# Optimization experiments

Hardware: AMD Instinct MI355X
Metric: run time of the kernel (lower is better)

## Reference

```python
import jax, jax.numpy as jnp
import numpy as np

B, S, E, H = 4, 2048, 1024, 4
D = E // H  # head_dim = 256


def setup_inputs() -> dict:
    key = jax.random.key(0)
    ks = jax.random.split(key, 9)
    scale = 1.0 / np.sqrt(E)
    return {
        "hidden_states": jax.random.normal(ks[0], (B, S, E), jnp.float32),
        "Wq": jax.random.normal(ks[1], (E, E), jnp.float32) * scale,
        "Wk": jax.random.normal(ks[2], (E, E), jnp.float32) * scale,
        "Wv": jax.random.normal(ks[3], (E, E), jnp.float32) * scale,
        "Wo": jax.random.normal(ks[4], (E, E), jnp.float32) * scale,
        "bo": jax.random.normal(ks[5], (E,), jnp.float32) * 0.02,
        "betas": jax.random.normal(ks[6], (1, H, 1, 1), jnp.float32),
        "mem": jax.random.uniform(ks[7], (H, D, D), jnp.float32),
        "z": jax.random.uniform(ks[8], (H, D, 1), jnp.float32),
    }


def _split_heads(t):  # [B,S,E] -> [B,H,S,D]
    return t.reshape(B, S, H, D).transpose(0, 2, 1, 3)


def reference(hidden_states, Wq, Wk, Wv, Wo, bo, betas, mem, z):
    q = _split_heads(hidden_states @ Wq)  # [B,H,S,D]
    k = _split_heads(hidden_states @ Wk)
    v = _split_heads(hidden_states @ Wv)

    # linear-attention feature map (ELU + 1)
    sigma_q = jax.nn.elu(q) + 1.0
    sigma_k = jax.nn.elu(k) + 1.0

    # compressive-memory read: mem [H,D,D], z [H,D,1] broadcast over batch
    A_mem = (sigma_q @ mem) / (sigma_q @ z + 1e-6)  # [B,H,S,D]

    # standard causal softmax attention
    attn_weights = jnp.einsum("bhqd,bhkd->bhqk", q, k)
    causal = jnp.tril(jnp.ones((S, S), bool))
    mask_value = jnp.finfo(attn_weights.dtype).min
    attn_weights = jnp.where(causal, attn_weights, mask_value)
    attn_weights = jax.nn.softmax(attn_weights, axis=-1)
    attn_output = jnp.einsum("bhqk,bhkd->bhqd", attn_weights, v)

    # per-head sigmoid gate mixing memory read and local attention
    gate = jax.nn.sigmoid(betas)  # [1,H,1,1]
    attn_output = gate * A_mem + (1.0 - gate) * attn_output

    # memory update (delta rule)
    delta = (sigma_k @ mem) / (sigma_k @ z + 1e-6)  # [B,H,S,D]
    mem_new = mem + jnp.einsum("bhsd,bhse->bhde", sigma_k, v - delta)  # [B,H,D,D]
    z_new = z + sigma_k.sum(axis=-2, keepdims=True).transpose(0, 1, 3, 2)  # [B,H,D,1]

    out = attn_output.transpose(0, 2, 1, 3).reshape(B, S, E) @ Wo + bo
    return out, mem_new, z_new
```

## Files before the change

kernel.cpp:

```cpp
#include <hip/hip_runtime.h>
#include <math.h>

#define Bn 4
#define Sn 2048
#define En 1024
#define Hn 4
#define Dn 256

typedef _Float16 half8 __attribute__((ext_vector_type(8)));
typedef _Float16 half4v __attribute__((ext_vector_type(4)));
typedef float floatx4 __attribute__((ext_vector_type(4)));

#define MFMA16(a, b, c) __builtin_amdgcn_mfma_f32_16x16x32_f16((a), (b), (c), 0, 0, 0)

__device__ __forceinline__ float elup1(float x) {
    return x > 0.0f ? x + 1.0f : __expf(x);
}

__global__ void cvt_h_k(const float* __restrict__ src, _Float16* __restrict__ dst, int n4) {
    int idx = blockIdx.x * 256 + threadIdx.x;
    const int stride = gridDim.x * 256;
    for (; idx < n4; idx += stride) {
        float4 v = ((const float4*)src)[idx];
        half4v o;
        o[0] = (_Float16)v.x; o[1] = (_Float16)v.y;
        o[2] = (_Float16)v.z; o[3] = (_Float16)v.w;
        ((half4v*)dst)[idx] = o;
    }
}

__global__ __launch_bounds__(256) void trans_f32f16_k(
    const float* __restrict__ src, _Float16* __restrict__ dst, int R, int C) {
    __shared__ float T[64][65];
    const int tid = threadIdx.x;
    const int c0 = blockIdx.x * 64, r0 = blockIdx.y * 64;
    src += (size_t)blockIdx.z * R * C;
    dst += (size_t)blockIdx.z * R * C;
    {
        const int tr = tid >> 2, tc = (tid & 3) * 16;
        const float* s = src + (size_t)(r0 + tr) * C + c0 + tc;
        #pragma unroll
        for (int i = 0; i < 4; ++i) {
            float4 v = *(const float4*)(s + i * 4);
            T[tr][tc + i * 4 + 0] = v.x;
            T[tr][tc + i * 4 + 1] = v.y;
            T[tr][tc + i * 4 + 2] = v.z;
            T[tr][tc + i * 4 + 3] = v.w;
        }
    }
    __syncthreads();
    {
        const int cr = tid >> 2, rc = (tid & 3) * 16;
        half8 h0, h1;
        #pragma unroll
        for (int i = 0; i < 8; ++i) h0[i] = (_Float16)T[rc + i][cr];
        #pragma unroll
        for (int i = 0; i < 8; ++i) h1[i] = (_Float16)T[rc + 8 + i][cr];
        _Float16* d = dst + (size_t)(c0 + cr) * R + r0 + rc;
        *(half8*)d = h0;
        *(half8*)(d + 8) = h1;
    }
}

__global__ __launch_bounds__(256) void trans_h16_k(
    const _Float16* __restrict__ Vh, _Float16* __restrict__ Vtg) {
    __shared__ __align__(16) unsigned short T[64 * 72];
    const int tid = threadIdx.x;
    const int s0 = blockIdx.x * 64;
    const int e0 = blockIdx.y * 64;
    const int b = blockIdx.z;
    const int h = e0 >> 8, d0 = e0 & 255;
    {
        const int tr = tid >> 2, tc = (tid & 3) * 16;
        const _Float16* s = Vh + (size_t)(b * Sn + s0 + tr) * En + e0 + tc;
        _Float16* d = (_Float16*)T + tr * 72 + tc;
        *(half8*)d = *(const half8*)s;
        *(half8*)(d + 8) = *(const half8*)(s + 8);
    }
    __syncthreads();
    {
        const int dr = tid >> 2, sc = (tid & 3) * 16;
        const _Float16* Tp = (const _Float16*)T;
        half8 h0, h1;
        #pragma unroll
        for (int i = 0; i < 8; ++i) h0[i] = Tp[(sc + i) * 72 + dr];
        #pragma unroll
        for (int i = 0; i < 8; ++i) h1[i] = Tp[(sc + 8 + i) * 72 + dr];
        _Float16* d = Vtg + (size_t)((b * 4 + h) * 256 + d0 + dr) * (size_t)Sn + s0 + sc;
        *(half8*)d = h0;
        *(half8*)(d + 8) = h1;
    }
}

__global__ __launch_bounds__(256) void gemm16_k(
    const _Float16* __restrict__ A, const _Float16* __restrict__ Bt,
    _Float16* __restrict__ C16, float* __restrict__ C32,
    const float* __restrict__ bias) {
    __shared__ __align__(16) unsigned short Ah[128 * 40];
    __shared__ __align__(16) unsigned short Bh[128 * 40];
    const int tid = threadIdx.x;
    const int lane = tid & 63, w = tid >> 6, quad = lane >> 4, l15 = lane & 15;
    const int bm = blockIdx.y * 128, bn = blockIdx.x * 128;
    floatx4 acc[2][8];
    #pragma unroll
    for (int mt = 0; mt < 2; ++mt)
        #pragma unroll
        for (int nt = 0; nt < 8; ++nt) acc[mt][nt] = (floatx4){0.f, 0.f, 0.f, 0.f};

    const int srow = tid >> 1, skoff = (tid & 1) * 16;
    const _Float16* as = A + (size_t)(bm + srow) * 1024 + skoff;
    const _Float16* bs = Bt + (size_t)(bn + srow) * 1024 + skoff;
    _Float16* ad = (_Float16*)Ah + srow * 40 + skoff;
    _Float16* bd = (_Float16*)Bh + srow * 40 + skoff;

    for (int k0 = 0; k0 < 1024; k0 += 32) {
        if (k0) __syncthreads();
        *(half8*)ad = *(const half8*)(as + k0);
        *(half8*)(ad + 8) = *(const half8*)(as + k0 + 8);
        *(half8*)bd = *(const half8*)(bs + k0);
        *(half8*)(bd + 8) = *(const half8*)(bs + k0 + 8);
        __syncthreads();
        half8 af0 = *(const half8*)((const _Float16*)Ah + (w * 32 + l15) * 40 + quad * 8);
        half8 af1 = *(const half8*)((const _Float16*)Ah + (w * 32 + 16 + l15) * 40 + quad * 8);
        #pragma unroll
        for (int nt = 0; nt < 8; ++nt) {
            half8 bf = *(const half8*)((const _Float16*)Bh + (nt * 16 + l15) * 40 + quad * 8);
            acc[0][nt] = MFMA16(af0, bf, acc[0][nt]);
            acc[1][nt] = MFMA16(af1, bf, acc[1][nt]);
        }
    }
    #pragma unroll
    for (int mt = 0; mt < 2; ++mt)
        #pragma unroll
        for (int nt = 0; nt < 8; ++nt)
            #pragma unroll
            for (int r = 0; r < 4; ++r) {
                const int row = bm + w * 32 + mt * 16 + quad * 4 + r;
                const int col = bn + nt * 16 + l15;
                if (C16)
                    C16[(size_t)row * 1024 + col] = (_Float16)acc[mt][nt][r];
                else
                    C32[(size_t)row * 1024 + col] = acc[mt][nt][r] + bias[col];
            }
}

__global__ __launch_bounds__(256) void flash_gate_k(
    const _Float16* __restrict__ Qh, const _Float16* __restrict__ Khg,
    const _Float16* __restrict__ Vtg, const _Float16* __restrict__ memT,
    const float* __restrict__ zp, const float* __restrict__ betas,
    _Float16* __restrict__ Cmb) {
    __shared__ __align__(16) unsigned short Ksh[32 * 264];
    __shared__ __align__(16) unsigned short Vt[256 * 40];
    __shared__ __align__(16) unsigned short Pb[4 * 16 * 40];

    const int tid = threadIdx.x;
    const int lane = tid & 63;
    const int w = tid >> 6;
    const int quad = lane >> 4;
    const int l15 = lane & 15;
    const int qt = 31 - blockIdx.x;
    const int bh = blockIdx.y;
    const int b = bh >> 2;
    const int h = bh & 3;
    const int q0 = qt * 64;

    const _Float16* Qrow = Qh + (size_t)(b * Sn + q0 + w * 16 + l15) * En + h * Dn;
    half8 qf[8], sf[8];
    float denp = 0.0f;
    #pragma unroll
    for (int kc = 0; kc < 8; ++kc) {
        half8 qv = *(const half8*)(Qrow + kc * 32 + quad * 8);
        qf[kc] = qv;
        const float* zb = zp + h * Dn + kc * 32 + quad * 8;
        float4 z0 = *(const float4*)zb;
        float4 z1 = *(const float4*)(zb + 4);
        float zz[8] = {z0.x, z0.y, z0.z, z0.w, z1.x, z1.y, z1.z, z1.w};
        half8 sv;
        #pragma unroll
        for (int j = 0; j < 8; ++j) {
            float s = elup1((float)qv[j]);
            sv[j] = (_Float16)s;
            denp += s * zz[j];
        }
        sf[kc] = sv;
    }
    denp += __shfl_xor(denp, 16);
    denp += __shfl_xor(denp, 32);
    const float deninv = 1.0f / (denp + 1e-6f);
    float den4[4];
    #pragma unroll
    for (int r = 0; r < 4; ++r) den4[r] = __shfl(deninv, quad * 4 + r);

    floatx4 acc[16];
    #pragma unroll
    for (int nt = 0; nt < 16; ++nt) acc[nt] = (floatx4){0.f, 0.f, 0.f, 0.f};

    const _Float16* memh = memT + (size_t)h * 256 * 256;
    for (int dc = 0; dc < 8; ++dc) {
        __syncthreads();
        {
            const _Float16* src = memh + (size_t)tid * 256 + dc * 32;
            _Float16* dst = (_Float16*)Vt + tid * 40;
            #pragma unroll
            for (int u = 0; u < 4; ++u) *(half8*)(dst + u * 8) = *(const half8*)(src + u * 8);
        }
        __syncthreads();
        #pragma unroll
        for (int nt = 0; nt < 16; ++nt) {
            half8 bm = *(const half8*)((const _Float16*)Vt + (nt * 16 + l15) * 40 + quad * 8);
            acc[nt] = MFMA16(sf[dc], bm, acc[nt]);
        }
    }

    const float gate = 1.0f / (1.0f + __expf(-betas[h]));
    const float omg = 1.0f - gate;
    _Float16* Cb = Cmb + (size_t)(b * Sn + q0 + w * 16) * En + h * Dn;
    #pragma unroll
    for (int nt = 0; nt < 16; ++nt)
        #pragma unroll
        for (int r = 0; r < 4; ++r) {
            Cb[(size_t)(quad * 4 + r) * En + nt * 16 + l15] =
                (_Float16)(gate * acc[nt][r] * den4[r]);
            acc[nt][r] = 0.0f;
        }

    float mold[4] = {-1e30f, -1e30f, -1e30f, -1e30f};
    float lsum[4] = {0.f, 0.f, 0.f, 0.f};
    float alpha[4];
    const _Float16* Kbase = Khg + (size_t)(b * Sn) * En + h * Dn;
    const _Float16* Vtb = Vtg + (size_t)bh * 256 * (size_t)Sn;
    const int ktend = 2 * qt + 1;
    for (int kt = 0; kt <= ktend; ++kt) {
        const int k0 = kt * 32;
        __syncthreads();
        {
            const int r = tid >> 3, doff = (tid & 7) * 32;
            const _Float16* src = Kbase + (size_t)(k0 + r) * En + doff;
            _Float16* dst = (_Float16*)Ksh + r * 264 + doff;
            #pragma unroll
            for (int u = 0; u < 4; ++u) *(half8*)(dst + u * 8) = *(const half8*)(src + u * 8);
        }
        {
            const _Float16* src = Vtb + (size_t)tid * Sn + k0;
            _Float16* dst = (_Float16*)Vt + tid * 40;
            #pragma unroll
            for (int u = 0; u < 4; ++u) *(half8*)(dst + u * 8) = *(const half8*)(src + u * 8);
        }
        __syncthreads();

        floatx4 S[2];
        S[0] = (floatx4){0.f, 0.f, 0.f, 0.f};
        S[1] = (floatx4){0.f, 0.f, 0.f, 0.f};
        #pragma unroll
        for (int kc = 0; kc < 8; ++kc) {
            half8 kf0 = *(const half8*)((const _Float16*)Ksh + l15 * 264 + kc * 32 + quad * 8);
            half8 kf1 = *(const half8*)((const _Float16*)Ksh + (16 + l15) * 264 + kc * 32 + quad * 8);
            S[0] = MFMA16(qf[kc], kf0, S[0]);
            S[1] = MFMA16(qf[kc], kf1, S[1]);
        }
        if (kt >= 2 * qt) {
            #pragma unroll
            for (int nt = 0; nt < 2; ++nt)
                #pragma unroll
                for (int r = 0; r < 4; ++r) {
                    const int kg = k0 + nt * 16 + l15;
                    const int qg = q0 + w * 16 + quad * 4 + r;
                    if (kg > qg) S[nt][r] = -1e30f;
                }
        }
        #pragma unroll
        for (int r = 0; r < 4; ++r) {
            float mx = fmaxf(S[0][r], S[1][r]);
            mx = fmaxf(mx, __shfl_xor(mx, 1));
            mx = fmaxf(mx, __shfl_xor(mx, 2));
            mx = fmaxf(mx, __shfl_xor(mx, 4));
            mx = fmaxf(mx, __shfl_xor(mx, 8));
            const float mnew = fmaxf(mold[r], mx);
            alpha[r] = __expf(mold[r] - mnew);
            mold[r] = mnew;
            const float p0 = __expf(S[0][r] - mnew);
            const float p1 = __expf(S[1][r] - mnew);
            float ps = p0 + p1;
            ps += __shfl_xor(ps, 1);
            ps += __shfl_xor(ps, 2);
            ps += __shfl_xor(ps, 4);
            ps += __shfl_xor(ps, 8);
            lsum[r] = lsum[r] * alpha[r] + ps;
            _Float16* pr = (_Float16*)Pb + (w * 16 + quad * 4 + r) * 40;
            pr[l15] = (_Float16)p0;
            pr[16 + l15] = (_Float16)p1;
        }
        #pragma unroll
        for (int nt = 0; nt < 16; ++nt)
            #pragma unroll
            for (int r = 0; r < 4; ++r) acc[nt][r] *= alpha[r];
        __syncthreads();
        half8 pf = *(const half8*)((const _Float16*)Pb + (w * 16 + l15) * 40 + quad * 8);
        #pragma unroll
        for (int nt = 0; nt < 16; ++nt) {
            half8 vf = *(const half8*)((const _Float16*)Vt + (nt * 16 + l15) * 40 + quad * 8);
            acc[nt] = MFMA16(pf, vf, acc[nt]);
        }
    }

    #pragma unroll
    for (int r = 0; r < 4; ++r) alpha[r] = omg / lsum[r];
    #pragma unroll
    for (int nt = 0; nt < 16; ++nt)
        #pragma unroll
        for (int r = 0; r < 4; ++r) {
            const size_t idx = (size_t)(quad * 4 + r) * En + nt * 16 + l15;
            const float prev = (float)Cb[idx];
            Cb[idx] = (_Float16)(prev + acc[nt][r] * alpha[r]);
        }
}

__global__ __launch_bounds__(256) void delta_v_k(
    const _Float16* __restrict__ Kg, _Float16* __restrict__ Vg,
    const float* __restrict__ memp, const float* __restrict__ zp) {
    __shared__ float SK[32][256];
    __shared__ float rden[32];
    const int tid = threadIdx.x;
    const int st = blockIdx.x;
    const int h = blockIdx.y;
    const int b = blockIdx.z;
    const int s0 = st * 32;
    const _Float16* Kb = Kg + (size_t)(b * Sn + s0) * En + h * Dn;
    _Float16* Vb = Vg + (size_t)(b * Sn + s0) * En + h * Dn;
    const float* memh = memp + (size_t)h * Dn * Dn;
    const float* zh = zp + (size_t)h * Dn;

    {
        const int lr = tid >> 3, ld = (tid & 7) * 32;
        const _Float16* kr = Kb + (size_t)lr * En + ld;
        #pragma unroll
        for (int u = 0; u < 4; ++u) {
            half8 k8 = *(const half8*)(kr + u * 8);
            #pragma unroll
            for (int j = 0; j < 8; ++j) SK[lr][ld + u * 8 + j] = elup1((float)k8[j]);
        }
    }
    __syncthreads();
    {
        const int r = tid >> 3;
        const int sl = (tid & 7) << 5;
        float part = 0.0f;
        #pragma unroll 8
        for (int d = 0; d < 32; ++d) part += SK[r][sl + d] * zh[sl + d];
        part += __shfl_down(part, 4);
        part += __shfl_down(part, 2);
        part += __shfl_down(part, 1);
        if ((tid & 7) == 0) rden[r] = 1.0f / (part + 1e-6f);
    }
    __syncthreads();
    const int c0 = (tid & 63) << 2;
    const int rb = tid >> 6;
    float dl[8][4] = {};
    for (int kk = 0; kk < Dn; ++kk) {
        const float4 m4 = *(const float4*)(memh + (size_t)kk * Dn + c0);
        #pragma unroll
        for (int k = 0; k < 8; ++k) {
            const float sk = SK[rb + 4 * k][kk];
            dl[k][0] += sk * m4.x;
            dl[k][1] += sk * m4.y;
            dl[k][2] += sk * m4.z;
            dl[k][3] += sk * m4.w;
        }
    }
    #pragma unroll
    for (int k = 0; k < 8; ++k) {
        const int r = rb + 4 * k;
        const float rd = rden[r];
        _Float16* vp = Vb + (size_t)r * En + c0;
        half4v v4 = *(half4v*)vp;
        #pragma unroll
        for (int j = 0; j < 4; ++j) v4[j] = (_Float16)((float)v4[j] - dl[k][j] * rd);
        *(half4v*)vp = v4;
    }
}

__global__ __launch_bounds__(256) void mem_update_k(
    const _Float16* __restrict__ Kg, const _Float16* __restrict__ U,
    const float* __restrict__ memp, float* __restrict__ mem_new) {
    __shared__ float As[16][64];
    __shared__ float Bs[16][64];
    const int tid = threadIdx.x;
    const int bn = blockIdx.x * 64;
    const int bm = blockIdx.y * 64;
    const int bh = blockIdx.z;
    const int b = bh >> 2;
    const int h = bh & 3;
    const _Float16* Kb = Kg + (size_t)b * Sn * En + h * Dn;
    const _Float16* Ub = U + (size_t)b * Sn * En + h * Dn;
    const int tr = tid >> 4, tc = tid & 15;
    const int lr = tid >> 4;
    const int lc = (tid & 15) << 2;
    float acc[4][4] = {};
    for (int s0 = 0; s0 < Sn; s0 += 16) {
        half4v a4 = *(const half4v*)(Kb + (size_t)(s0 + lr) * En + bm + lc);
        As[lr][lc + 0] = elup1((float)a4[0]);
        As[lr][lc + 1] = elup1((float)a4[1]);
        As[lr][lc + 2] = elup1((float)a4[2]);
        As[lr][lc + 3] = elup1((float)a4[3]);
        half4v b4 = *(const half4v*)(Ub + (size_t)(s0 + lr) * En + bn + lc);
        Bs[lr][lc + 0] = (float)b4[0];
        Bs[lr][lc + 1] = (float)b4[1];
        Bs[lr][lc + 2] = (float)b4[2];
        Bs[lr][lc + 3] = (float)b4[3];
        __syncthreads();
        #pragma unroll
        for (int kk = 0; kk < 16; ++kk) {
            float a[4], bb[4];
            #pragma unroll
            for (int i = 0; i < 4; ++i) a[i] = As[kk][tr * 4 + i];
            #pragma unroll
            for (int j = 0; j < 4; ++j) bb[j] = Bs[kk][tc * 4 + j];
            #pragma unroll
            for (int i = 0; i < 4; ++i)
                #pragma unroll
                for (int j = 0; j < 4; ++j)
                    acc[i][j] += a[i] * bb[j];
        }
        __syncthreads();
    }
    const float* memh = memp + (size_t)h * Dn * Dn;
    float* mout = mem_new + (size_t)bh * Dn * Dn;
    #pragma unroll
    for (int i = 0; i < 4; ++i) {
        const int dm = bm + tr * 4 + i;
        const float4 m4 = *(const float4*)(memh + (size_t)dm * Dn + bn + tc * 4);
        float4 r;
        r.x = m4.x + acc[i][0];
        r.y = m4.y + acc[i][1];
        r.z = m4.z + acc[i][2];
        r.w = m4.w + acc[i][3];
        *(float4*)(mout + (size_t)dm * Dn + bn + tc * 4) = r;
    }
}

__global__ __launch_bounds__(256) void znew_init_k(
    const float* __restrict__ zp, float* __restrict__ z_new) {
    const int bh = blockIdx.x;
    const int h = bh & 3;
    z_new[(size_t)bh * Dn + threadIdx.x] = zp[(size_t)h * Dn + threadIdx.x];
}

__global__ __launch_bounds__(256) void znew_acc_k(
    const _Float16* __restrict__ Kg, float* __restrict__ z_new) {
    const int bh = blockIdx.y;
    const int b = bh >> 2;
    const int h = bh & 3;
    const int s0 = blockIdx.x * 256;
    const _Float16* Kb = Kg + (size_t)(b * Sn + s0) * En + h * Dn;
    float acc = 0.0f;
    for (int s = 0; s < 256; ++s) acc += elup1((float)Kb[(size_t)s * En + threadIdx.x]);
    atomicAdd(&z_new[(size_t)bh * Dn + threadIdx.x], acc);
}

extern "C" void kernel_launch(void* const* d_in, const int* in_sizes, int n_in,
                              void* d_out, int out_size, void* d_ws, size_t ws_size,
                              hipStream_t stream) {
    const float* hidden = (const float*)d_in[0];
    const float* Wq = (const float*)d_in[1];
    const float* Wk = (const float*)d_in[2];
    const float* Wv = (const float*)d_in[3];
    const float* Wo = (const float*)d_in[4];
    const float* bo = (const float*)d_in[5];
    const float* betas = (const float*)d_in[6];
    const float* memp = (const float*)d_in[7];
    const float* zp = (const float*)d_in[8];

    float* out = (float*)d_out;
    float* mem_new = out + (size_t)Bn * Sn * En;
    float* z_new = mem_new + (size_t)Bn * Hn * Dn * Dn;

    _Float16* p = (_Float16*)d_ws;
    const size_t BSE = (size_t)Bn * Sn * En;
    _Float16* hh   = p; p += BSE;
    _Float16* Qh   = p; p += BSE;
    _Float16* Kh   = p; p += BSE;
    _Float16* Vh   = p; p += BSE;
    _Float16* Vtg  = p; p += BSE;
    _Float16* Cmb  = p; p += BSE;
    _Float16* WqT  = p; p += (size_t)En * En;
    _Float16* WkT  = p; p += (size_t)En * En;
    _Float16* WvT  = p; p += (size_t)En * En;
    _Float16* WoT  = p; p += (size_t)En * En;
    _Float16* memT = p; p += (size_t)Hn * Dn * Dn;

    cvt_h_k<<<2048, 256, 0, stream>>>(hidden, hh, (int)(BSE / 4));
    trans_f32f16_k<<<dim3(16, 16, 1), 256, 0, stream>>>(Wq, WqT, En, En);
    trans_f32f16_k<<<dim3(16, 16, 1), 256, 0, stream>>>(Wk, WkT, En, En);
    trans_f32f16_k<<<dim3(16, 16, 1), 256, 0, stream>>>(Wv, WvT, En, En);
    trans_f32f16_k<<<dim3(16, 16, 1), 256, 0, stream>>>(Wo, WoT, En, En);
    trans_f32f16_k<<<dim3(4, 4, 4), 256, 0, stream>>>(memp, memT, Dn, Dn);

    gemm16_k<<<dim3(8, 64), 256, 0, stream>>>(hh, WqT, Qh, nullptr, nullptr);
    gemm16_k<<<dim3(8, 64), 256, 0, stream>>>(hh, WkT, Kh, nullptr, nullptr);
    gemm16_k<<<dim3(8, 64), 256, 0, stream>>>(hh, WvT, Vh, nullptr, nullptr);

    trans_h16_k<<<dim3(32, 16, 4), 256, 0, stream>>>(Vh, Vtg);

    flash_gate_k<<<dim3(32, 16), 256, 0, stream>>>(Qh, Kh, Vtg, memT, zp, betas, Cmb);

    delta_v_k<<<dim3(64, 4, 4), 256, 0, stream>>>(Kh, Vh, memp, zp);
    mem_update_k<<<dim3(4, 4, 16), 256, 0, stream>>>(Kh, Vh, memp, mem_new);

    znew_init_k<<<16, 256, 0, stream>>>(zp, z_new);
    znew_acc_k<<<dim3(8, 16), 256, 0, stream>>>(Kh, z_new);

    gemm16_k<<<dim3(8, 64), 256, 0, stream>>>(Cmb, WoT, nullptr, out, bo);
}
```

Measured before the change: 795.2 us.

## Split long causal flash rows across two blocks, fuse fp32 input conversion into GEMM

The longest query tiles in the causal flash kernel are split into two key-range units, and a new merge kernel combines their partial outputs using their max and sum statistics. This balances work across blocks and raises the number of blocks in flight. The separate hidden-state fp16 conversion kernel is dropped, and the QKV GEMMs now read fp32 directly and convert while staging into shared memory. The flash loop also register-prefetches the next K/V tile, replaces a barrier with an LDS wait, and sets a launch-bounds occupancy hint, at the cost of extra partial-output traffic and one more kernel launch.

```diff
diff --git a/kernel.cpp b/kernel.cpp
--- a/kernel.cpp
+++ b/kernel.cpp
@@ -15,18 +15,6 @@
 
 __device__ __forceinline__ float elup1(float x) {
     return x > 0.0f ? x + 1.0f : __expf(x);
-}
-
-__global__ void cvt_h_k(const float* __restrict__ src, _Float16* __restrict__ dst, int n4) {
-    int idx = blockIdx.x * 256 + threadIdx.x;
-    const int stride = gridDim.x * 256;
-    for (; idx < n4; idx += stride) {
-        float4 v = ((const float4*)src)[idx];
-        half4v o;
-        o[0] = (_Float16)v.x; o[1] = (_Float16)v.y;
-        o[2] = (_Float16)v.z; o[3] = (_Float16)v.w;
-        ((half4v*)dst)[idx] = o;
-    }
 }
 
 __global__ __launch_bounds__(256) void trans_f32f16_k(
@@ -92,8 +80,9 @@
     }
 }
 
+template <bool A32>
 __global__ __launch_bounds__(256) void gemm16_k(
-    const _Float16* __restrict__ A, const _Float16* __restrict__ Bt,
+    const void* __restrict__ Ap, const _Float16* __restrict__ Bt,
     _Float16* __restrict__ C16, float* __restrict__ C32,
     const float* __restrict__ bias) {
     __shared__ __align__(16) unsigned short Ah[128 * 40];
@@ -108,15 +97,32 @@
         for (int nt = 0; nt < 8; ++nt) acc[mt][nt] = (floatx4){0.f, 0.f, 0.f, 0.f};
 
     const int srow = tid >> 1, skoff = (tid & 1) * 16;
-    const _Float16* as = A + (size_t)(bm + srow) * 1024 + skoff;
     const _Float16* bs = Bt + (size_t)(bn + srow) * 1024 + skoff;
     _Float16* ad = (_Float16*)Ah + srow * 40 + skoff;
     _Float16* bd = (_Float16*)Bh + srow * 40 + skoff;
 
     for (int k0 = 0; k0 < 1024; k0 += 32) {
         if (k0) __syncthreads();
-        *(half8*)ad = *(const half8*)(as + k0);
-        *(half8*)(ad + 8) = *(const half8*)(as + k0 + 8);
+        if constexpr (A32) {
+            const float* as = (const float*)Ap + (size_t)(bm + srow) * 1024 + skoff + k0;
+            half8 h0, h1;
+            #pragma unroll
+            for (int i = 0; i < 2; ++i) {
+                float4 f0 = *(const float4*)(as + i * 8);
+                float4 f1 = *(const float4*)(as + i * 8 + 4);
+                half8* hp = i ? &h1 : &h0;
+                (*hp)[0] = (_Float16)f0.x; (*hp)[1] = (_Float16)f0.y;
+                (*hp)[2] = (_Float16)f0.z; (*hp)[3] = (_Float16)f0.w;
+                (*hp)[4] = (_Float16)f1.x; (*hp)[5] = (_Float16)f1.y;
+                (*hp)[6] = (_Float16)f1.z; (*hp)[7] = (_Float16)f1.w;
+            }
+            *(half8*)ad = h0;
+            *(half8*)(ad + 8) = h1;
+        } else {
+            const _Float16* as = (const _Float16*)Ap + (size_t)(bm + srow) * 1024 + skoff + k0;
+            *(half8*)ad = *(const half8*)as;
+            *(half8*)(ad + 8) = *(const half8*)(as + 8);
+        }
         *(half8*)bd = *(const half8*)(bs + k0);
         *(half8*)(bd + 8) = *(const half8*)(bs + k0 + 8);
         __syncthreads();
@@ -144,133 +150,153 @@
             }
 }
 
-__global__ __launch_bounds__(256) void flash_gate_k(
+__global__ __launch_bounds__(256, 3) void flash_gate_k(
     const _Float16* __restrict__ Qh, const _Float16* __restrict__ Khg,
     const _Float16* __restrict__ Vtg, const _Float16* __restrict__ memT,
     const float* __restrict__ zp, const float* __restrict__ betas,
-    _Float16* __restrict__ Cmb) {
+    _Float16* __restrict__ Cmb, _Float16* __restrict__ Opart,
+    float* __restrict__ mpart, float* __restrict__ lpart) {
     __shared__ __align__(16) unsigned short Ksh[32 * 264];
     __shared__ __align__(16) unsigned short Vt[256 * 40];
-    __shared__ __align__(16) unsigned short Pb[4 * 16 * 40];
+    __shared__ __align__(16) unsigned short Pb[64 * 40];
 
     const int tid = threadIdx.x;
     const int lane = tid & 63;
     const int w = tid >> 6;
     const int quad = lane >> 4;
     const int l15 = lane & 15;
-    const int qt = 31 - blockIdx.x;
+    const int bx = blockIdx.x;
     const int bh = blockIdx.y;
-    const int b = bh >> 2;
-    const int h = bh & 3;
+    const int b = bh >> 2, h = bh & 3;
+
+    int qt, kt0, kt1, unit;
+    if (bx < 32) {
+        qt = 31 - (bx >> 1);
+        unit = bx & 1;
+        kt0 = unit ? (qt + 1) : 0;
+        kt1 = unit ? (2 * qt + 2) : (qt + 1);
+    } else {
+        qt = 15 - (bx - 32);
+        unit = 0;
+        kt0 = 0;
+        kt1 = 2 * qt + 2;
+    }
+    const bool two = (bx < 32);
     const int q0 = qt * 64;
 
     const _Float16* Qrow = Qh + (size_t)(b * Sn + q0 + w * 16 + l15) * En + h * Dn;
-    half8 qf[8], sf[8];
-    float denp = 0.0f;
-    #pragma unroll
-    for (int kc = 0; kc < 8; ++kc) {
-        half8 qv = *(const half8*)(Qrow + kc * 32 + quad * 8);
-        qf[kc] = qv;
-        const float* zb = zp + h * Dn + kc * 32 + quad * 8;
-        float4 z0 = *(const float4*)zb;
-        float4 z1 = *(const float4*)(zb + 4);
-        float zz[8] = {z0.x, z0.y, z0.z, z0.w, z1.x, z1.y, z1.z, z1.w};
-        half8 sv;
-        #pragma unroll
-        for (int j = 0; j < 8; ++j) {
-            float s = elup1((float)qv[j]);
-            sv[j] = (_Float16)s;
-            denp += s * zz[j];
-        }
-        sf[kc] = sv;
-    }
-    denp += __shfl_xor(denp, 16);
-    denp += __shfl_xor(denp, 32);
-    const float deninv = 1.0f / (denp + 1e-6f);
-    float den4[4];
-    #pragma unroll
-    for (int r = 0; r < 4; ++r) den4[r] = __shfl(deninv, quad * 4 + r);
+    half8 qf[8];
+    #pragma unroll
+    for (int kc = 0; kc < 8; ++kc) qf[kc] = *(const half8*)(Qrow + kc * 32 + quad * 8);
 
     floatx4 acc[16];
     #pragma unroll
     for (int nt = 0; nt < 16; ++nt) acc[nt] = (floatx4){0.f, 0.f, 0.f, 0.f};
-
-    const _Float16* memh = memT + (size_t)h * 256 * 256;
-    for (int dc = 0; dc < 8; ++dc) {
-        __syncthreads();
-        {
-            const _Float16* src = memh + (size_t)tid * 256 + dc * 32;
-            _Float16* dst = (_Float16*)Vt + tid * 40;
-            #pragma unroll
-            for (int u = 0; u < 4; ++u) *(half8*)(dst + u * 8) = *(const half8*)(src + u * 8);
-        }
-        __syncthreads();
-        #pragma unroll
-        for (int nt = 0; nt < 16; ++nt) {
-            half8 bm = *(const half8*)((const _Float16*)Vt + (nt * 16 + l15) * 40 + quad * 8);
-            acc[nt] = MFMA16(sf[dc], bm, acc[nt]);
-        }
-    }
 
     const float gate = 1.0f / (1.0f + __expf(-betas[h]));
     const float omg = 1.0f - gate;
     _Float16* Cb = Cmb + (size_t)(b * Sn + q0 + w * 16) * En + h * Dn;
-    #pragma unroll
-    for (int nt = 0; nt < 16; ++nt)
-        #pragma unroll
-        for (int r = 0; r < 4; ++r) {
-            Cb[(size_t)(quad * 4 + r) * En + nt * 16 + l15] =
-                (_Float16)(gate * acc[nt][r] * den4[r]);
-            acc[nt][r] = 0.0f;
-        }
+    _Float16* KshF = (_Float16*)Ksh;
+    _Float16* VtF = (_Float16*)Vt;
+    _Float16* PbF = (_Float16*)Pb;
+
+    if (unit == 0) {
+        float denp = 0.0f;
+        const _Float16* memh = memT + (size_t)h * Dn * Dn;
+        for (int dc = 0; dc < 8; ++dc) {
+            __syncthreads();
+            {
+                const _Float16* src = memh + (size_t)tid * 256 + dc * 32;
+                _Float16* dst = VtF + tid * 40;
+                #pragma unroll
+                for (int u = 0; u < 4; ++u) *(half8*)(dst + u * 8) = *(const half8*)(src + u * 8);
+            }
+            __syncthreads();
+            half8 sv;
+            const float* zb = zp + h * Dn + dc * 32 + quad * 8;
+            #pragma unroll
+            for (int j = 0; j < 8; ++j) {
+                const float s = elup1((float)qf[dc][j]);
+                sv[j] = (_Float16)s;
+                denp += s * zb[j];
+            }
+            #pragma unroll
+            for (int nt = 0; nt < 16; ++nt) {
+                half8 bm = *(const half8*)(VtF + (nt * 16 + l15) * 40 + quad * 8);
+                acc[nt] = MFMA16(sv, bm, acc[nt]);
+            }
+        }
+        denp += __shfl_xor(denp, 16);
+        denp += __shfl_xor(denp, 32);
+        const float deninv = 1.0f / (denp + 1e-6f);
+        float den4[4];
+        #pragma unroll
+        for (int r = 0; r < 4; ++r) den4[r] = __shfl(deninv, quad * 4 + r);
+        #pragma unroll
+        for (int nt = 0; nt < 16; ++nt)
+            #pragma unroll
+            for (int r = 0; r < 4; ++r) {
+                Cb[(size_t)(quad * 4 + r) * En + nt * 16 + l15] =
+                    (_Float16)(gate * acc[nt][r] * den4[r]);
+                acc[nt][r] = 0.0f;
+            }
+    }
+
+    const _Float16* Kbase = Khg + (size_t)(b * Sn) * En + h * Dn;
+    const _Float16* Vtb = Vtg + (size_t)bh * 256 * (size_t)Sn;
+    const _Float16* kptr = Kbase + (size_t)(kt0 * 32 + (tid >> 3)) * En + (tid & 7) * 32;
+    const _Float16* vptr = Vtb + (size_t)tid * Sn + kt0 * 32;
+    half8 kr[4], vr[4];
+    #pragma unroll
+    for (int u = 0; u < 4; ++u) {
+        kr[u] = *(const half8*)(kptr + u * 8);
+        vr[u] = *(const half8*)(vptr + u * 8);
+    }
 
     float mold[4] = {-1e30f, -1e30f, -1e30f, -1e30f};
     float lsum[4] = {0.f, 0.f, 0.f, 0.f};
     float alpha[4];
-    const _Float16* Kbase = Khg + (size_t)(b * Sn) * En + h * Dn;
-    const _Float16* Vtb = Vtg + (size_t)bh * 256 * (size_t)Sn;
-    const int ktend = 2 * qt + 1;
-    for (int kt = 0; kt <= ktend; ++kt) {
+    const int krow_off = (tid >> 3) * 264 + (tid & 7) * 32;
+
+    for (int kt = kt0; kt < kt1; ++kt) {
         const int k0 = kt * 32;
         __syncthreads();
-        {
-            const int r = tid >> 3, doff = (tid & 7) * 32;
-            const _Float16* src = Kbase + (size_t)(k0 + r) * En + doff;
-            _Float16* dst = (_Float16*)Ksh + r * 264 + doff;
-            #pragma unroll
-            for (int u = 0; u < 4; ++u) *(half8*)(dst + u * 8) = *(const half8*)(src + u * 8);
-        }
-        {
-            const _Float16* src = Vtb + (size_t)tid * Sn + k0;
-            _Float16* dst = (_Float16*)Vt + tid * 40;
-            #pragma unroll
-            for (int u = 0; u < 4; ++u) *(half8*)(dst + u * 8) = *(const half8*)(src + u * 8);
+        #pragma unroll
+        for (int u = 0; u < 4; ++u) {
+            *(half8*)(KshF + krow_off + u * 8) = kr[u];
+            *(half8*)(VtF + tid * 40 + u * 8) = vr[u];
         }
         __syncthreads();
-
-        floatx4 S[2];
-        S[0] = (floatx4){0.f, 0.f, 0.f, 0.f};
-        S[1] = (floatx4){0.f, 0.f, 0.f, 0.f};
+        if (kt + 1 < kt1) {
+            kptr += 32 * En;
+            vptr += 32;
+            #pragma unroll
+            for (int u = 0; u < 4; ++u) {
+                kr[u] = *(const half8*)(kptr + u * 8);
+                vr[u] = *(const half8*)(vptr + u * 8);
+            }
+        }
+
+        floatx4 S0 = (floatx4){0.f, 0.f, 0.f, 0.f};
+        floatx4 S1 = (floatx4){0.f, 0.f, 0.f, 0.f};
         #pragma unroll
         for (int kc = 0; kc < 8; ++kc) {
-            half8 kf0 = *(const half8*)((const _Float16*)Ksh + l15 * 264 + kc * 32 + quad * 8);
-            half8 kf1 = *(const half8*)((const _Float16*)Ksh + (16 + l15) * 264 + kc * 32 + quad * 8);
-            S[0] = MFMA16(qf[kc], kf0, S[0]);
-            S[1] = MFMA16(qf[kc], kf1, S[1]);
+            half8 kf0 = *(const half8*)(KshF + l15 * 264 + kc * 32 + quad * 8);
+            half8 kf1 = *(const half8*)(KshF + (16 + l15) * 264 + kc * 32 + quad * 8);
+            S0 = MFMA16(qf[kc], kf0, S0);
+            S1 = MFMA16(qf[kc], kf1, S1);
         }
         if (kt >= 2 * qt) {
             #pragma unroll
-            for (int nt = 0; nt < 2; ++nt)
-                #pragma unroll
-                for (int r = 0; r < 4; ++r) {
-                    const int kg = k0 + nt * 16 + l15;
-                    const int qg = q0 + w * 16 + quad * 4 + r;
-                    if (kg > qg) S[nt][r] = -1e30f;
-                }
+            for (int r = 0; r < 4; ++r) {
+                const int qg = q0 + w * 16 + quad * 4 + r;
+                if (k0 + l15 > qg) S0[r] = -1e30f;
+                if (k0 + 16 + l15 > qg) S1[r] = -1e30f;
+            }
         }
         #pragma unroll
         for (int r = 0; r < 4; ++r) {
-            float mx = fmaxf(S[0][r], S[1][r]);
+            float mx = fmaxf(S0[r], S1[r]);
             mx = fmaxf(mx, __shfl_xor(mx, 1));
             mx = fmaxf(mx, __shfl_xor(mx, 2));
             mx = fmaxf(mx, __shfl_xor(mx, 4));
@@ -278,41 +304,94 @@
             const float mnew = fmaxf(mold[r], mx);
             alpha[r] = __expf(mold[r] - mnew);
             mold[r] = mnew;
-            const float p0 = __expf(S[0][r] - mnew);
-            const float p1 = __expf(S[1][r] - mnew);
+            const float p0 = __expf(S0[r] - mnew);
+            const float p1 = __expf(S1[r] - mnew);
             float ps = p0 + p1;
             ps += __shfl_xor(ps, 1);
             ps += __shfl_xor(ps, 2);
             ps += __shfl_xor(ps, 4);
             ps += __shfl_xor(ps, 8);
             lsum[r] = lsum[r] * alpha[r] + ps;
-            _Float16* pr = (_Float16*)Pb + (w * 16 + quad * 4 + r) * 40;
+            _Float16* pr = PbF + (w * 16 + quad * 4 + r) * 40;
             pr[l15] = (_Float16)p0;
             pr[16 + l15] = (_Float16)p1;
         }
         #pragma unroll
+        for (int nt = 0; nt < 16; ++nt) {
+            acc[nt][0] *= alpha[0];
+            acc[nt][1] *= alpha[1];
+            acc[nt][2] *= alpha[2];
+            acc[nt][3] *= alpha[3];
+        }
+        __asm__ volatile("s_waitcnt lgkmcnt(0)" ::: "memory");
+        half8 pf = *(const half8*)(PbF + (w * 16 + l15) * 40 + quad * 8);
+        #pragma unroll
+        for (int nt = 0; nt < 16; ++nt) {
+            half8 vf = *(const half8*)(VtF + (nt * 16 + l15) * 40 + quad * 8);
+            acc[nt] = MFMA16(pf, vf, acc[nt]);
+        }
+    }
+
+    if (!two) {
+        #pragma unroll
+        for (int r = 0; r < 4; ++r) alpha[r] = omg / lsum[r];
+        #pragma unroll
         for (int nt = 0; nt < 16; ++nt)
             #pragma unroll
-            for (int r = 0; r < 4; ++r) acc[nt][r] *= alpha[r];
-        __syncthreads();
-        half8 pf = *(const half8*)((const _Float16*)Pb + (w * 16 + l15) * 40 + quad * 8);
-        #pragma unroll
-        for (int nt = 0; nt < 16; ++nt) {
-            half8 vf = *(const half8*)((const _Float16*)Vt + (nt * 16 + l15) * 40 + quad * 8);
-            acc[nt] = MFMA16(pf, vf, acc[nt]);
-        }
-    }
-
-    #pragma unroll
-    for (int r = 0; r < 4; ++r) alpha[r] = omg / lsum[r];
-    #pragma unroll
-    for (int nt = 0; nt < 16; ++nt)
-        #pragma unroll
-        for (int r = 0; r < 4; ++r) {
-            const size_t idx = (size_t)(quad * 4 + r) * En + nt * 16 + l15;
-            const float prev = (float)Cb[idx];
-            Cb[idx] = (_Float16)(prev + acc[nt][r] * alpha[r]);
-        }
+            for (int r = 0; r < 4; ++r) {
+                const size_t idx = (size_t)(quad * 4 + r) * En + nt * 16 + l15;
+                Cb[idx] = (_Float16)((float)Cb[idx] + acc[nt][r] * alpha[r]);
+            }
+    } else {
+        const int pidx = ((qt - 16) * 16 + bh) * 2 + unit;
+        _Float16* Op = Opart + ((size_t)pidx * 64 + w * 16) * 256;
+        #pragma unroll
+        for (int nt = 0; nt < 16; ++nt)
+            #pragma unroll
+            for (int r = 0; r < 4; ++r)
+                Op[(quad * 4 + r) * 256 + nt * 16 + l15] = (_Float16)acc[nt][r];
+        if (l15 == 0) {
+            #pragma unroll
+            for (int r = 0; r < 4; ++r) {
+                mpart[pidx * 64 + w * 16 + quad * 4 + r] = mold[r];
+                lpart[pidx * 64 + w * 16 + quad * 4 + r] = lsum[r];
+            }
+        }
+    }
+}
+
+__global__ __launch_bounds__(256) void merge_k(
+    const _Float16* __restrict__ Opart, const float* __restrict__ mpart,
+    const float* __restrict__ lpart, const float* __restrict__ betas,
+    _Float16* __restrict__ Cmb) {
+    const int qi = blockIdx.x;
+    const int bh = blockIdx.y;
+    const int b = bh >> 2, h = bh & 3;
+    const int tid = threadIdx.x;
+    const int idx = (qi * 16 + bh) * 2;
+    const float gate = 1.0f / (1.0f + __expf(-betas[h]));
+    const float omg = 1.0f - gate;
+    const int rsub = tid >> 6;
+    const int c0 = (tid & 63) * 4;
+    const _Float16* O0 = Opart + (size_t)idx * 64 * 256;
+    const _Float16* O1 = O0 + 64 * 256;
+    const int q0 = (16 + qi) * 64;
+    for (int chunk = 0; chunk < 16; ++chunk) {
+        const int r = chunk * 4 + rsub;
+        const float m0 = mpart[idx * 64 + r], l0 = lpart[idx * 64 + r];
+        const float m1 = mpart[(idx + 1) * 64 + r], l1 = lpart[(idx + 1) * 64 + r];
+        const float mm = fmaxf(m0, m1);
+        const float s0 = __expf(m0 - mm), s1 = __expf(m1 - mm);
+        const float rl = omg / (l0 * s0 + l1 * s1);
+        half4v o0 = *(const half4v*)(O0 + r * 256 + c0);
+        half4v o1 = *(const half4v*)(O1 + r * 256 + c0);
+        _Float16* cp = Cmb + (size_t)(b * Sn + q0 + r) * En + h * Dn + c0;
+        half4v cv = *(half4v*)cp;
+        #pragma unroll
+        for (int j = 0; j < 4; ++j)
+            cv[j] = (_Float16)((float)cv[j] + ((float)o0[j] * s0 + (float)o1[j] * s1) * rl);
+        *(half4v*)cp = cv;
+    }
 }
 
 __global__ __launch_bounds__(256) void delta_v_k(
@@ -474,34 +553,38 @@
     float* mem_new = out + (size_t)Bn * Sn * En;
     float* z_new = mem_new + (size_t)Bn * Hn * Dn * Dn;
 
+    const size_t BSE = (size_t)Bn * Sn * En;
     _Float16* p = (_Float16*)d_ws;
-    const size_t BSE = (size_t)Bn * Sn * En;
-    _Float16* hh   = p; p += BSE;
-    _Float16* Qh   = p; p += BSE;
-    _Float16* Kh   = p; p += BSE;
-    _Float16* Vh   = p; p += BSE;
-    _Float16* Vtg  = p; p += BSE;
-    _Float16* Cmb  = p; p += BSE;
-    _Float16* WqT  = p; p += (size_t)En * En;
-    _Float16* WkT  = p; p += (size_t)En * En;
-    _Float16* WvT  = p; p += (size_t)En * En;
-    _Float16* WoT  = p; p += (size_t)En * En;
-    _Float16* memT = p; p += (size_t)Hn * Dn * Dn;
-
-    cvt_h_k<<<2048, 256, 0, stream>>>(hidden, hh, (int)(BSE / 4));
+    _Float16* Qh = p;    p += BSE;
+    _Float16* Kh = p;    p += BSE;
+    _Float16* Vh = p;    p += BSE;
+    _Float16* Vtg = p;   p += BSE;
+    _Float16* Cmb = p;   p += BSE;
+    _Float16* Opart = p; p += (size_t)512 * 64 * 256;
+    _Float16* WqT = p;   p += (size_t)En * En;
+    _Float16* WkT = p;   p += (size_t)En * En;
+    _Float16* WvT = p;   p += (size_t)En * En;
+    _Float16* WoT = p;   p += (size_t)En * En;
+    _Float16* memT = p;  p += (size_t)Hn * Dn * Dn;
+    float* fp = (float*)p;
+    float* mpart = fp;   fp += 512 * 64;
+    float* lpart = fp;   fp += 512 * 64;
+
     trans_f32f16_k<<<dim3(16, 16, 1), 256, 0, stream>>>(Wq, WqT, En, En);
     trans_f32f16_k<<<dim3(16, 16, 1), 256, 0, stream>>>(Wk, WkT, En, En);
     trans_f32f16_k<<<dim3(16, 16, 1), 256, 0, stream>>>(Wv, WvT, En, En);
     trans_f32f16_k<<<dim3(16, 16, 1), 256, 0, stream>>>(Wo, WoT, En, En);
     trans_f32f16_k<<<dim3(4, 4, 4), 256, 0, stream>>>(memp, memT, Dn, Dn);
 
-    gemm16_k<<<dim3(8, 64), 256, 0, stream>>>(hh, WqT, Qh, nullptr, nullptr);
-    gemm16_k<<<dim3(8, 64), 256, 0, stream>>>(hh, WkT, Kh, nullptr, nullptr);
-    gemm16_k<<<dim3(8, 64), 256, 0, stream>>>(hh, WvT, Vh, nullptr, nullptr);
+    gemm16_k<true><<<dim3(8, 64), 256, 0, stream>>>(hidden, WqT, Qh, nullptr, nullptr);
+    gemm16_k<true><<<dim3(8, 64), 256, 0, stream>>>(hidden, WkT, Kh, nullptr, nullptr);
+    gemm16_k<true><<<dim3(8, 64), 256, 0, stream>>>(hidden, WvT, Vh, nullptr, nullptr);
 
     trans_h16_k<<<dim3(32, 16, 4), 256, 0, stream>>>(Vh, Vtg);
 
-    flash_gate_k<<<dim3(32, 16), 256, 0, stream>>>(Qh, Kh, Vtg, memT, zp, betas, Cmb);
+    flash_gate_k<<<dim3(48, 16), 256, 0, stream>>>(
+        Qh, Kh, Vtg, memT, zp, betas, Cmb, Opart, mpart, lpart);
+    merge_k<<<dim3(16, 16), 256, 0, stream>>>(Opart, mpart, lpart, betas, Cmb);
 
     delta_v_k<<<dim3(64, 4, 4), 256, 0, stream>>>(Kh, Vh, memp, zp);
     mem_update_k<<<dim3(4, 4, 16), 256, 0, stream>>>(Kh, Vh, memp, mem_new);
@@ -509,5 +592,5 @@
     znew_init_k<<<16, 256, 0, stream>>>(zp, z_new);
     znew_acc_k<<<dim3(8, 16), 256, 0, stream>>>(Kh, z_new);
 
-    gemm16_k<<<dim3(8, 64), 256, 0, stream>>>(Cmb, WoT, nullptr, out, bo);
-}
+    gemm16_k<false><<<dim3(8, 64), 256, 0, stream>>>(Cmb, WoT, nullptr, out, bo);
+}
```

New measurement: 651.5 us. -18.1%, faster.
